# Performance work log

Measured on AMD Instinct MI355X. Metric: run time of the kernel, lower is better.

Reference implementation:

```python
import jax, jax.numpy as jnp
import numpy as np

B, N, D, DG = 32, 2048, 512, 1024


def layernorm(x, g, b, eps=1e-5):
    m = jnp.mean(x, axis=-1, keepdims=True)
    v = jnp.mean((x - m) ** 2, axis=-1, keepdims=True)
    return (x - m) * jax.lax.rsqrt(v + eps) * g + b


def simple_rms_norm(x, eps=1e-6):
    # parameter-free RMSNorm used inside Hgru1d
    return x * jax.lax.rsqrt(jnp.mean(x * x, axis=-1, keepdims=True) + eps)


def linear_recurrence(lam, u, reverse):
    # h_t = lam_t * h_{t-1} + u_t along axis=1, via associative scan
    def comb(c1, c2):
        a1, b1 = c1
        a2, b2 = c2
        return a1 * a2, a2 * b1 + b2
    return jax.lax.associative_scan(comb, (lam, u), axis=1, reverse=reverse)[1]


def hgru1d(x, lower_bound, Wi, bi, Wf, bf, Wg, bg, Wo, bo):
    # HGRN-style gated recurrence, bidirectional (causal=False, shared params)
    i = jax.nn.silu(x @ Wi + bi)                       # candidate input  [b,n,d]
    f = jax.nn.sigmoid(x @ Wf + bf)                    # forget gate      [b,n,d]
    lam = lower_bound + (1.0 - lower_bound) * f        # lower-bounded decay
    u = (1.0 - lam) * i
    h = linear_recurrence(lam, u, False) + linear_recurrence(lam, u, True)
    h = simple_rms_norm(h)
    g = jax.nn.sigmoid(x @ Wg + bg)                    # output gate
    return (h * g) @ Wo + bo


def glu(x, W1, b1, W2, b2, W3, b3):
    return (jax.nn.silu(x @ W1 + b1) * (x @ W2 + b2)) @ W3 + b3


def setup_inputs() -> dict:
    key = jax.random.key(0)
    ks = jax.random.split(key, 16)
    s = 0.02
    return {
        "x": jax.random.normal(ks[0], (B, N, D), dtype=jnp.float32),
        "lower_bound": 0,
        "Wi": jax.random.normal(ks[1], (D, D), jnp.float32) * s,
        "bi": jnp.zeros((D,), jnp.float32),
        "Wf": jax.random.normal(ks[2], (D, D), jnp.float32) * s,
        "bf": jnp.zeros((D,), jnp.float32),
        "Wg": jax.random.normal(ks[3], (D, D), jnp.float32) * s,
        "bg": jnp.zeros((D,), jnp.float32),
        "Wo": jax.random.normal(ks[4], (D, D), jnp.float32) * s,
        "bo": jnp.zeros((D,), jnp.float32),
        "tn_g": jnp.ones((D,), jnp.float32),
        "tn_b": jnp.zeros((D,), jnp.float32),
        "fn_g": jnp.ones((D,), jnp.float32),
        "fn_b": jnp.zeros((D,), jnp.float32),
        "W1": jax.random.normal(ks[5], (D, DG), jnp.float32) * s,
        "b1": jnp.zeros((DG,), jnp.float32),
        "W2": jax.random.normal(ks[6], (D, DG), jnp.float32) * s,
        "b2": jnp.zeros((DG,), jnp.float32),
        "W3": jax.random.normal(ks[7], (DG, D), jnp.float32) * s,
        "b3": jnp.zeros((D,), jnp.float32),
    }


def reference(x, lower_bound, Wi, bi, Wf, bf, Wg, bg, Wo, bo,
              tn_g, tn_b, fn_g, fn_b, W1, b1, W2, b2, W3, b3):
    lb = jnp.float32(lower_bound)
    # post-norm residual block
    x = x + layernorm(hgru1d(x, lb, Wi, bi, Wf, bf, Wg, bg, Wo, bo), tn_g, tn_b)
    x = x + layernorm(glu(x, W1, b1, W2, b2, W3, b3), fn_g, fn_b)
    return x
```

## Files before the change

kernel.cpp:

```cpp
#include <hip/hip_runtime.h>
#include <hip/hip_bf16.h>

#define BB 32
#define NN 2048
#define DD 512
#define DGG 1024
#define CC 32
#define LLEN 64

typedef short bf16x8 __attribute__((ext_vector_type(8)));
typedef float f32x4  __attribute__((ext_vector_type(4)));

__device__ __forceinline__ unsigned short f2bf(float f){
    __hip_bfloat16 h = __float2bfloat16(f);
    return *reinterpret_cast<unsigned short*>(&h);
}
__device__ __forceinline__ float bf2f(unsigned short u){
    unsigned int x = ((unsigned int)u) << 16;
    return __uint_as_float(x);
}
__device__ __forceinline__ float sigm(float x){ return 1.0f/(1.0f + __expf(-x)); }

__device__ __forceinline__ void gl_lds16(const unsigned short* g, unsigned short* l){
    __builtin_amdgcn_global_load_lds(
        (const __attribute__((address_space(1))) unsigned int*)g,
        (__attribute__((address_space(3))) unsigned int*)l, 16, 0, 0);
}

__global__ __launch_bounds__(256)
void wt_prep(const float* __restrict__ in, unsigned short* __restrict__ out,
             int K, int N)
{
    __shared__ float t[32][33];
    const int tid = threadIdx.x;
    const int r = tid >> 3;
    const int c = (tid & 7) << 2;
    const int n0 = blockIdx.x * 32;
    const int k0 = blockIdx.y * 32;
    float4 v = *(const float4*)(in + (size_t)(k0 + r) * N + n0 + c);
    t[r][c] = v.x; t[r][c+1] = v.y; t[r][c+2] = v.z; t[r][c+3] = v.w;
    __syncthreads();
    ushort4 o;
    o.x = f2bf(t[c+0][r]); o.y = f2bf(t[c+1][r]);
    o.z = f2bf(t[c+2][r]); o.w = f2bf(t[c+3][r]);
    *(ushort4*)(out + (size_t)(n0 + r) * K + k0 + c) = o;
}

__global__ __launch_bounds__(256)
void wt_prep_pair(const float* __restrict__ in0, const float* __restrict__ in1,
                  unsigned short* __restrict__ out, int K, int N)
{
    __shared__ float t[32][33];
    const int tid = threadIdx.x;
    const int bx  = blockIdx.x;
    const int k0  = blockIdx.y * 32;
    const int kk  = tid >> 3;
    const int rq  = (tid & 7) << 2;
    const float* src = ((rq >> 4) & 1) ? in1 : in0;
    const int c0 = bx * 16 + (rq & 15);
    float4 v = *(const float4*)(src + (size_t)(k0 + kk) * N + c0);
    t[kk][rq] = v.x; t[kk][rq+1] = v.y; t[kk][rq+2] = v.z; t[kk][rq+3] = v.w;
    __syncthreads();
    const int rr = tid >> 3;
    const int kc = (tid & 7) << 2;
    ushort4 o;
    o.x = f2bf(t[kc+0][rr]); o.y = f2bf(t[kc+1][rr]);
    o.z = f2bf(t[kc+2][rr]); o.w = f2bf(t[kc+3][rr]);
    *(ushort4*)(out + (size_t)(bx * 32 + rr) * K + k0 + kc) = o;
}

__global__ __launch_bounds__(256)
void cast_bf16(const float* __restrict__ in, unsigned short* __restrict__ out)
{
    size_t i = ((size_t)blockIdx.x * 256 + threadIdx.x) * 4;
    float4 v = *(const float4*)(in + i);
    ushort4 o;
    o.x = f2bf(v.x); o.y = f2bf(v.y); o.z = f2bf(v.z); o.w = f2bf(v.w);
    *(ushort4*)(out + i) = o;
}

template<int MODE, int K, int NI>
__global__ __launch_bounds__(512, 2)
void gemm8p(const unsigned short* __restrict__ A,
            const unsigned short* __restrict__ Bt,
            const float* __restrict__ bias0,
            const float* __restrict__ bias1,
            unsigned short* __restrict__ out0,
            unsigned short* __restrict__ out1,
            const int* __restrict__ lbp, int Mtiles)
{
    constexpr int NKT   = K / 64;
    constexpr int ITERS = NKT / 2;
    constexpr int Ntl   = NI / 256;
    constexpr int NOUT  = (MODE >= 5) ? NI / 2 : NI;
    __shared__ unsigned short As0[256*64], As1[256*64];
    __shared__ unsigned short Bs0[256*64], Bs1[256*64];

    const int tid  = threadIdx.x;
    const int wave = tid >> 6;
    const int lane = tid & 63;
    const int lm   = lane & 15;
    const int quad = lane >> 4;
    const int wr   = (wave >> 2) * 128;
    const int wc   = (wave & 3) * 64;

    const int nwg = Mtiles * Ntl;
    const int hb  = blockIdx.x;
    const int wg  = (hb & 7) * (nwg >> 3) + (hb >> 3);
    const int bm  = wg / Ntl;
    const int bn  = wg - bm * Ntl;
    const size_t m0 = (size_t)bm * 256;
    const int    n0 = bn * 256;

    const int r8 = lane >> 3;
    const int sl = (lane & 7) ^ r8;
    const unsigned short* gA = A  + (m0 + wave * 8 + r8) * (size_t)K + sl * 8;
    const unsigned short* gB = Bt + ((size_t)n0 + wave * 8 + r8) * K + sl * 8;
    const int ldw = wave * 8 * 64;
    const int sx  = lm & 7;

#define STG(XS, gX, kt, hh) do {                                              \
        gl_lds16(gX + (size_t)((hh)*128)      * K + (kt)*64,                  \
                 XS + ((hh)*128)      * 64 + ldw);                            \
        gl_lds16(gX + (size_t)((hh)*128 + 64) * K + (kt)*64,                  \
                 XS + ((hh)*128 + 64) * 64 + ldw);                            \
    } while (0)

#define MFQ(mh, nh, bsel) do {                                                \
        _Pragma("unroll") for (int ks = 0; ks < 2; ++ks)                      \
        _Pragma("unroll") for (int mi = 0; mi < 4; ++mi)                      \
        _Pragma("unroll") for (int ni = 0; ni < 2; ++ni)                      \
            acc[(mh)*4+mi][(nh)*2+ni] = __builtin_amdgcn_mfma_f32_16x16x32_bf16( \
                a[mi][ks], bsel[ni][ks], acc[(mh)*4+mi][(nh)*2+ni], 0, 0, 0); \
    } while (0)

#define RD_A(XS, mh) do {                                                     \
        _Pragma("unroll") for (int ks = 0; ks < 2; ++ks)                      \
        _Pragma("unroll") for (int mi = 0; mi < 4; ++mi)                      \
            a[mi][ks] = *(const bf16x8*)&XS[(wr + ((mh)*4+mi)*16 + lm)*64     \
                                            + ((ks*4+quad) ^ sx)*8];          \
    } while (0)
#define RD_B(XS, nh, breg) do {                                               \
        _Pragma("unroll") for (int ks = 0; ks < 2; ++ks)                      \
        _Pragma("unroll") for (int ni = 0; ni < 2; ++ni)                      \
            breg[ni][ks] = *(const bf16x8*)&XS[(wc + ((nh)*2+ni)*16 + lm)*64  \
                                               + ((ks*4+quad) ^ sx)*8];       \
    } while (0)

#define BARRIER()  __builtin_amdgcn_s_barrier()
#define LGKM0()    asm volatile("s_waitcnt lgkmcnt(0)" ::: "memory")
#define VMC(n)     asm volatile("s_waitcnt vmcnt(" #n ")" ::: "memory")

    f32x4 acc[8][4];
    #pragma unroll
    for (int i = 0; i < 8; ++i)
        #pragma unroll
        for (int j = 0; j < 4; ++j) acc[i][j] = (f32x4){0.f, 0.f, 0.f, 0.f};

    bf16x8 a[4][2], bA[2][2], bB[2][2];

    STG(Bs0, gB, 0, 0); STG(As0, gA, 0, 0); STG(As0, gA, 0, 1);
    STG(Bs0, gB, 0, 1); STG(Bs1, gB, 1, 0); STG(As1, gA, 1, 0);
    VMC(4);
    BARRIER();

    #pragma unroll
    for (int j = 0; j < ITERS; ++j) {
        const bool LAST = (j == ITERS - 1);
        RD_A(As0, 0); RD_B(Bs0, 0, bA);
        STG(As1, gA, 2*j + 1, 1);
        BARRIER(); LGKM0();
        __builtin_amdgcn_s_setprio(1); MFQ(0, 0, bA); __builtin_amdgcn_s_setprio(0);
        BARRIER();
        RD_B(Bs0, 1, bB);
        STG(Bs1, gB, 2*j + 1, 1);
        BARRIER(); LGKM0();
        __builtin_amdgcn_s_setprio(1); MFQ(0, 1, bB); __builtin_amdgcn_s_setprio(0);
        BARRIER();
        RD_A(As0, 1);
        if (2*j + 2 < NKT) STG(Bs0, gB, 2*j + 2, 0);
        BARRIER(); LGKM0();
        __builtin_amdgcn_s_setprio(1); MFQ(1, 0, bA); __builtin_amdgcn_s_setprio(0);
        BARRIER();
        if (2*j + 2 < NKT) STG(As0, gA, 2*j + 2, 0);
        BARRIER(); LGKM0();
        __builtin_amdgcn_s_setprio(1); MFQ(1, 1, bB); __builtin_amdgcn_s_setprio(0);
        if (LAST) { VMC(0); } else { VMC(4); }
        BARRIER();
        RD_A(As1, 0); RD_B(Bs1, 0, bA);
        if (2*j + 2 < NKT) STG(As0, gA, 2*j + 2, 1);
        BARRIER(); LGKM0();
        __builtin_amdgcn_s_setprio(1); MFQ(0, 0, bA); __builtin_amdgcn_s_setprio(0);
        BARRIER();
        RD_B(Bs1, 1, bB);
        if (2*j + 2 < NKT) STG(Bs0, gB, 2*j + 2, 1);
        BARRIER(); LGKM0();
        __builtin_amdgcn_s_setprio(1); MFQ(0, 1, bB); __builtin_amdgcn_s_setprio(0);
        BARRIER();
        RD_A(As1, 1);
        if (2*j + 3 < NKT) STG(Bs1, gB, 2*j + 3, 0);
        BARRIER(); LGKM0();
        __builtin_amdgcn_s_setprio(1); MFQ(1, 0, bA); __builtin_amdgcn_s_setprio(0);
        BARRIER();
        if (2*j + 3 < NKT) STG(As1, gA, 2*j + 3, 0);
        BARRIER(); LGKM0();
        __builtin_amdgcn_s_setprio(1); MFQ(1, 1, bB); __builtin_amdgcn_s_setprio(0);
        if (!LAST) { VMC(4); BARRIER(); }
    }
#undef STG
#undef MFQ
#undef RD_A
#undef RD_B
#undef BARRIER
#undef LGKM0
#undef VMC

    float lbv = 0.f;
    if constexpr (MODE == 5) lbv = (float)(*lbp);

    if constexpr (MODE == 5 || MODE == 6) {
        const int cbase = (n0 + wc) >> 1;
        #pragma unroll
        for (int nip = 0; nip < 4; nip += 2) {
            const int c = cbase + (nip >> 1) * 16 + lm;
            const float b0 = bias0[c];
            const float b1v = bias1[c];
            #pragma unroll
            for (int mi = 0; mi < 8; ++mi) {
                #pragma unroll
                for (int r = 0; r < 4; ++r) {
                    const size_t row = m0 + wr + mi * 16 + quad * 4 + r;
                    const size_t oidx = row * NOUT + c;
                    float p0 = acc[mi][nip][r]     + b0;
                    float p1 = acc[mi][nip + 1][r] + b1v;
                    if constexpr (MODE == 5) {
                        float si = p0 * sigm(p0);
                        float fv = sigm(p1);
                        float lamv = lbv + (1.f - lbv) * fv;
                        out0[oidx] = f2bf(lamv);
                        out1[oidx] = f2bf((1.f - lamv) * si);
                    } else {
                        out0[oidx] = f2bf(p0 * sigm(p0) * p1);
                    }
                }
            }
        }
    } else {
        #pragma unroll
        for (int ni = 0; ni < 4; ++ni) {
            const int col = n0 + wc + ni * 16 + lm;
            const float bcol = bias0[col];
            #pragma unroll
            for (int mi = 0; mi < 8; ++mi) {
                #pragma unroll
                for (int r = 0; r < 4; ++r) {
                    const size_t row = m0 + wr + mi * 16 + quad * 4 + r;
                    const size_t oidx = row * NOUT + col;
                    float v = acc[mi][ni][r] + bcol;
                    if constexpr (MODE == 0) out0[oidx] = f2bf(v);
                    else                     out0[oidx] = f2bf(sigm(v));
                }
            }
        }
    }
}

__global__ __launch_bounds__(512)
void scan_agg(const unsigned short* __restrict__ lam, const unsigned short* __restrict__ u,
              float* __restrict__ Aarr, float* __restrict__ Vf, float* __restrict__ Vr)
{
    int bc = blockIdx.x;
    int b = bc >> 5, c = bc & 31;
    int d = threadIdx.x;
    size_t base = ((size_t)b * NN + c * LLEN) * DD + d;
    float A = 1.f, vf = 0.f, vr = 0.f;
    for (int t = 0; t < LLEN; ++t) {
        float lv = bf2f(lam[base + (size_t)t * DD]);
        float uv = bf2f(u[base + (size_t)t * DD]);
        vf = lv * vf + uv;
        vr += uv * A;
        A *= lv;
    }
    size_t o = (size_t)bc * DD + d;
    Aarr[o] = A; Vf[o] = vf; Vr[o] = vr;
}

__global__ __launch_bounds__(256)
void scan_comb(const float* __restrict__ Aarr, const float* __restrict__ Vf,
               const float* __restrict__ Vr, float* __restrict__ cf, float* __restrict__ cr)
{
    int g = blockIdx.x * 256 + threadIdx.x;
    int b = g >> 9, d = g & 511;
    float S = 0.f;
    for (int c = 0; c < CC; ++c) {
        size_t o = (size_t)(b * CC + c) * DD + d;
        cf[o] = S;
        S = Vf[o] + Aarr[o] * S;
    }
    S = 0.f;
    for (int c = CC - 1; c >= 0; --c) {
        size_t o = (size_t)(b * CC + c) * DD + d;
        cr[o] = S;
        S = Vr[o] + Aarr[o] * S;
    }
}

__global__ __launch_bounds__(256)
void scan_final(const unsigned short* __restrict__ lam, const unsigned short* __restrict__ u,
                const float* __restrict__ cf, const float* __restrict__ cr,
                float* __restrict__ h)
{
    int bid = blockIdx.x;
    int dh = bid & 1, c = (bid >> 1) & 31, b = bid >> 6;
    int d = dh * 256 + threadIdx.x;
    size_t base = ((size_t)b * NN + c * LLEN) * DD + d;
    size_t co   = (size_t)(b * CC + c) * DD + d;

    float hbuf[LLEN];
    float hf = cf[co];
    #pragma unroll
    for (int t = 0; t < LLEN; ++t) {
        float lv = bf2f(lam[base + (size_t)t * DD]);
        float uv = bf2f(u[base + (size_t)t * DD]);
        hf = lv * hf + uv;
        hbuf[t] = hf;
    }
    float hr = cr[co];
    #pragma unroll
    for (int t = LLEN - 1; t >= 0; --t) {
        float lv = bf2f(lam[base + (size_t)t * DD]);
        float uv = bf2f(u[base + (size_t)t * DD]);
        hr = lv * hr + uv;
        h[base + (size_t)t * DD] = hbuf[t] + hr;
    }
}

__global__ __launch_bounds__(256)
void rms_mul(const float* __restrict__ h, const unsigned short* __restrict__ g,
             unsigned short* __restrict__ hg)
{
    int row = blockIdx.x;
    size_t base = (size_t)row * DD;
    int tid = threadIdx.x, col = tid * 2;
    float2 v = *(const float2*)&h[base + col];
    float ss = v.x * v.x + v.y * v.y;
    #pragma unroll
    for (int off = 32; off > 0; off >>= 1) ss += __shfl_down(ss, off);
    __shared__ float ps[4];
    __shared__ float scale_s;
    if ((tid & 63) == 0) ps[tid >> 6] = ss;
    __syncthreads();
    if (tid == 0) scale_s = rsqrtf((ps[0] + ps[1] + ps[2] + ps[3]) * (1.f / DD) + 1e-6f);
    __syncthreads();
    float sc = scale_s;
    ushort2 gv = *(const ushort2*)&g[base + col];
    ushort2 o;
    o.x = f2bf(v.x * sc * bf2f(gv.x));
    o.y = f2bf(v.y * sc * bf2f(gv.y));
    *(ushort2*)&hg[base + col] = o;
}

__global__ __launch_bounds__(256)
void add_ln(const float* __restrict__ xin, const unsigned short* __restrict__ y,
            const float* __restrict__ gam, const float* __restrict__ bet,
            float* __restrict__ out, unsigned short* __restrict__ outb)
{
    int row = blockIdx.x;
    size_t base = (size_t)row * DD;
    int tid = threadIdx.x, col = tid * 2;
    ushort2 yv = *(const ushort2*)&y[base + col];
    float vx = bf2f(yv.x), vy = bf2f(yv.y);
    float s = vx + vy;
    float ss = vx * vx + vy * vy;
    #pragma unroll
    for (int off = 32; off > 0; off >>= 1) {
        s  += __shfl_down(s, off);
        ss += __shfl_down(ss, off);
    }
    __shared__ float ps[8];
    __shared__ float stats[2];
    if ((tid & 63) == 0) { ps[tid >> 6] = s; ps[4 + (tid >> 6)] = ss; }
    __syncthreads();
    if (tid == 0) {
        float st  = ps[0] + ps[1] + ps[2] + ps[3];
        float sst = ps[4] + ps[5] + ps[6] + ps[7];
        float mean = st * (1.f / DD);
        float var  = sst * (1.f / DD) - mean * mean;
        stats[0] = mean; stats[1] = rsqrtf(var + 1e-5f);
    }
    __syncthreads();
    float mean = stats[0], inv = stats[1];
    float2 xv = *(const float2*)&xin[base + col];
    float2 gv = *(const float2*)&gam[col];
    float2 bv = *(const float2*)&bet[col];
    float2 o;
    o.x = xv.x + (vx - mean) * inv * gv.x + bv.x;
    o.y = xv.y + (vy - mean) * inv * gv.y + bv.y;
    *(float2*)&out[base + col] = o;
    if (outb) {
        ushort2 ob; ob.x = f2bf(o.x); ob.y = f2bf(o.y);
        *(ushort2*)&outb[base + col] = ob;
    }
}

extern "C" void kernel_launch(void* const* d_in, const int* in_sizes, int n_in,
                              void* d_out, int out_size, void* d_ws, size_t ws_size,
                              hipStream_t stream)
{
    const float* x   = (const float*)d_in[0];
    const int*   lb  = (const int*)d_in[1];
    const float* Wi  = (const float*)d_in[2];
    const float* bi  = (const float*)d_in[3];
    const float* Wf  = (const float*)d_in[4];
    const float* bfp = (const float*)d_in[5];
    const float* Wg  = (const float*)d_in[6];
    const float* bg  = (const float*)d_in[7];
    const float* Wo  = (const float*)d_in[8];
    const float* bo  = (const float*)d_in[9];
    const float* tng = (const float*)d_in[10];
    const float* tnb = (const float*)d_in[11];
    const float* fng = (const float*)d_in[12];
    const float* fnb = (const float*)d_in[13];
    const float* W1  = (const float*)d_in[14];
    const float* b1  = (const float*)d_in[15];
    const float* W2  = (const float*)d_in[16];
    const float* b2  = (const float*)d_in[17];
    const float* W3  = (const float*)d_in[18];
    const float* b3  = (const float*)d_in[19];

    unsigned short* wbase = (unsigned short*)d_ws;
    unsigned short* WifT = wbase;
    unsigned short* WgT  = WifT + 524288;
    unsigned short* WoT  = WgT + 262144;
    unsigned short* W12T = WoT + 262144;
    unsigned short* W3T  = W12T + 1048576;
    const size_t WTOT = 524288 + 262144 + 262144 + 1048576 + 524288;

    wt_prep_pair<<<dim3(32, 16), 256, 0, stream>>>(Wi, Wf, WifT, 512, 512);
    wt_prep<<<dim3(16, 16), 256, 0, stream>>>(Wg, WgT, 512, 512);
    wt_prep<<<dim3(16, 16), 256, 0, stream>>>(Wo, WoT, 512, 512);
    wt_prep_pair<<<dim3(64, 16), 256, 0, stream>>>(W1, W2, W12T, 512, 1024);
    wt_prep<<<dim3(16, 32), 256, 0, stream>>>(W3, W3T, 1024, 512);

    const size_t perB = (size_t)4 * NN * DD * 2 + (size_t)5 * CC * DD * 4;
    int Bch = 32;
    while (Bch > 1 && WTOT * 2 + (size_t)Bch * perB > ws_size) Bch >>= 1;
    const int nch = BB / Bch;

    const size_t slabE = (size_t)Bch * NN * DD;

    for (int ch = 0; ch < nch; ++ch) {
        const size_t r0 = (size_t)ch * Bch * NN;
        const int Mc = Bch * NN;
        const int Mt = Mc / 256;
        const float* xc = x + r0 * DD;
        unsigned short* S0 = wbase + WTOT;
        unsigned short* S1 = S0 + slabE;
        unsigned short* S2 = S0 + 2 * slabE;
        unsigned short* S3 = S0 + 3 * slabE;
        float* small = (float*)(S0 + 4 * slabE);
        const size_t agg = (size_t)Bch * CC * DD;
        float* Aarr = small;
        float* VfP  = small + agg;
        float* VrP  = small + 2 * agg;
        float* cfP  = small + 3 * agg;
        float* crP  = small + 4 * agg;
        float* hout = (float*)d_out + r0 * DD;

        cast_bf16<<<Mc / 2, 256, 0, stream>>>(xc, S3);
        gemm8p<5, 512, 1024><<<Mt * 4, 512, 0, stream>>>(
            S3, WifT, bi, bfp, S1, S0, lb, Mt);
        gemm8p<2, 512, 512><<<Mt * 2, 512, 0, stream>>>(
            S3, WgT, bg, nullptr, S2, nullptr, nullptr, Mt);
        scan_agg<<<Bch * CC, 512, 0, stream>>>(S1, S0, Aarr, VfP, VrP);
        scan_comb<<<(Bch * DD) / 256, 256, 0, stream>>>(Aarr, VfP, VrP, cfP, crP);
        scan_final<<<Bch * CC * 2, 256, 0, stream>>>(S1, S0, cfP, crP, hout);
        rms_mul<<<Mc, 256, 0, stream>>>(hout, S2, S2);
        gemm8p<0, 512, 512><<<Mt * 2, 512, 0, stream>>>(
            S2, WoT, bo, nullptr, S0, nullptr, nullptr, Mt);
        add_ln<<<Mc, 256, 0, stream>>>(xc, S0, tng, tnb, hout, S3);
        gemm8p<6, 512, 2048><<<Mt * 8, 512, 0, stream>>>(
            S3, W12T, b1, b2, S1, nullptr, nullptr, Mt);
        gemm8p<0, 1024, 512><<<Mt * 2, 512, 0, stream>>>(
            S1, W3T, b3, nullptr, S0, nullptr, nullptr, Mt);
        add_ln<<<Mc, 256, 0, stream>>>(hout, S0, fng, fnb, hout, nullptr);
    }
}
```

Before: 1.115 ms.

## Make GEMM blocks loop over several consecutive N tiles sharing one M row

New measurement: 1.504 ms. 1.35x slower.

```diff
diff --git a/kernel.cpp b/kernel.cpp
--- a/kernel.cpp
+++ b/kernel.cpp
@@ -87,7 +87,7 @@
             const float* __restrict__ bias1,
             unsigned short* __restrict__ out0,
             unsigned short* __restrict__ out1,
-            const int* __restrict__ lbp, int Mtiles)
+            const int* __restrict__ lbp, int TPB)
 {
     constexpr int NKT   = K / 64;
     constexpr int ITERS = NKT / 2;
@@ -104,18 +104,15 @@
     const int wr   = (wave >> 2) * 128;
     const int wc   = (wave & 3) * 64;
 
-    const int nwg = Mtiles * Ntl;
-    const int hb  = blockIdx.x;
-    const int wg  = (hb & 7) * (nwg >> 3) + (hb >> 3);
-    const int bm  = wg / Ntl;
-    const int bn  = wg - bm * Ntl;
+    const int start = blockIdx.x * TPB;
+    const int bm  = start / Ntl;
+    const int bn0 = start - bm * Ntl;
     const size_t m0 = (size_t)bm * 256;
-    const int    n0 = bn * 256;
 
     const int r8 = lane >> 3;
     const int sl = (lane & 7) ^ r8;
     const unsigned short* gA = A  + (m0 + wave * 8 + r8) * (size_t)K + sl * 8;
-    const unsigned short* gB = Bt + ((size_t)n0 + wave * 8 + r8) * K + sl * 8;
+    const unsigned short* gB = Bt + ((size_t)bn0 * 256 + wave * 8 + r8) * K + sl * 8;
     const int ldw = wave * 8 * 64;
     const int sx  = lm & 7;
 
@@ -152,60 +149,115 @@
 #define VMC(n)     asm volatile("s_waitcnt vmcnt(" #n ")" ::: "memory")
 
     f32x4 acc[8][4];
-    #pragma unroll
-    for (int i = 0; i < 8; ++i)
+    bf16x8 a[4][2], bA[2][2], bB[2][2];
+
+    float lbv = 0.f;
+    if constexpr (MODE == 5) lbv = (float)(*lbp);
+
+    #pragma unroll 1
+    for (int t = 0; t < TPB; ++t) {
         #pragma unroll
-        for (int j = 0; j < 4; ++j) acc[i][j] = (f32x4){0.f, 0.f, 0.f, 0.f};
-
-    bf16x8 a[4][2], bA[2][2], bB[2][2];
-
-    STG(Bs0, gB, 0, 0); STG(As0, gA, 0, 0); STG(As0, gA, 0, 1);
-    STG(Bs0, gB, 0, 1); STG(Bs1, gB, 1, 0); STG(As1, gA, 1, 0);
-    VMC(4);
-    BARRIER();
-
-    #pragma unroll
-    for (int j = 0; j < ITERS; ++j) {
-        const bool LAST = (j == ITERS - 1);
-        RD_A(As0, 0); RD_B(Bs0, 0, bA);
-        STG(As1, gA, 2*j + 1, 1);
-        BARRIER(); LGKM0();
-        __builtin_amdgcn_s_setprio(1); MFQ(0, 0, bA); __builtin_amdgcn_s_setprio(0);
+        for (int i = 0; i < 8; ++i)
+            #pragma unroll
+            for (int jj = 0; jj < 4; ++jj) acc[i][jj] = (f32x4){0.f, 0.f, 0.f, 0.f};
+
+        STG(Bs0, gB, 0, 0); STG(As0, gA, 0, 0); STG(As0, gA, 0, 1);
+        STG(Bs0, gB, 0, 1); STG(Bs1, gB, 1, 0); STG(As1, gA, 1, 0);
+        VMC(4);
         BARRIER();
-        RD_B(Bs0, 1, bB);
-        STG(Bs1, gB, 2*j + 1, 1);
-        BARRIER(); LGKM0();
-        __builtin_amdgcn_s_setprio(1); MFQ(0, 1, bB); __builtin_amdgcn_s_setprio(0);
-        BARRIER();
-        RD_A(As0, 1);
-        if (2*j + 2 < NKT) STG(Bs0, gB, 2*j + 2, 0);
-        BARRIER(); LGKM0();
-        __builtin_amdgcn_s_setprio(1); MFQ(1, 0, bA); __builtin_amdgcn_s_setprio(0);
-        BARRIER();
-        if (2*j + 2 < NKT) STG(As0, gA, 2*j + 2, 0);
-        BARRIER(); LGKM0();
-        __builtin_amdgcn_s_setprio(1); MFQ(1, 1, bB); __builtin_amdgcn_s_setprio(0);
-        if (LAST) { VMC(0); } else { VMC(4); }
-        BARRIER();
-        RD_A(As1, 0); RD_B(Bs1, 0, bA);
-        if (2*j + 2 < NKT) STG(As0, gA, 2*j + 2, 1);
-        BARRIER(); LGKM0();
-        __builtin_amdgcn_s_setprio(1); MFQ(0, 0, bA); __builtin_amdgcn_s_setprio(0);
-        BARRIER();
-        RD_B(Bs1, 1, bB);
-        if (2*j + 2 < NKT) STG(Bs0, gB, 2*j + 2, 1);
-        BARRIER(); LGKM0();
-        __builtin_amdgcn_s_setprio(1); MFQ(0, 1, bB); __builtin_amdgcn_s_setprio(0);
-        BARRIER();
-        RD_A(As1, 1);
-        if (2*j + 3 < NKT) STG(Bs1, gB, 2*j + 3, 0);
-        BARRIER(); LGKM0();
-        __builtin_amdgcn_s_setprio(1); MFQ(1, 0, bA); __builtin_amdgcn_s_setprio(0);
-        BARRIER();
-        if (2*j + 3 < NKT) STG(As1, gA, 2*j + 3, 0);
-        BARRIER(); LGKM0();
-        __builtin_amdgcn_s_setprio(1); MFQ(1, 1, bB); __builtin_amdgcn_s_setprio(0);
-        if (!LAST) { VMC(4); BARRIER(); }
+
+        #pragma unroll
+        for (int j = 0; j < ITERS; ++j) {
+            const bool JL = (j == ITERS - 1);
+            RD_A(As0, 0); RD_B(Bs0, 0, bA);
+            STG(As1, gA, 2*j + 1, 1);
+            BARRIER(); LGKM0();
+            __builtin_amdgcn_s_setprio(1); MFQ(0, 0, bA); __builtin_amdgcn_s_setprio(0);
+            BARRIER();
+            RD_B(Bs0, 1, bB);
+            STG(Bs1, gB, 2*j + 1, 1);
+            BARRIER(); LGKM0();
+            __builtin_amdgcn_s_setprio(1); MFQ(0, 1, bB); __builtin_amdgcn_s_setprio(0);
+            BARRIER();
+            RD_A(As0, 1);
+            if (2*j + 2 < NKT) STG(Bs0, gB, 2*j + 2, 0);
+            BARRIER(); LGKM0();
+            __builtin_amdgcn_s_setprio(1); MFQ(1, 0, bA); __builtin_amdgcn_s_setprio(0);
+            BARRIER();
+            if (2*j + 2 < NKT) STG(As0, gA, 2*j + 2, 0);
+            BARRIER(); LGKM0();
+            __builtin_amdgcn_s_setprio(1); MFQ(1, 1, bB); __builtin_amdgcn_s_setprio(0);
+            if (JL) { VMC(0); } else { VMC(4); }
+            BARRIER();
+            RD_A(As1, 0); RD_B(Bs1, 0, bA);
+            if (2*j + 2 < NKT) STG(As0, gA, 2*j + 2, 1);
+            BARRIER(); LGKM0();
+            __builtin_amdgcn_s_setprio(1); MFQ(0, 0, bA); __builtin_amdgcn_s_setprio(0);
+            BARRIER();
+            RD_B(Bs1, 1, bB);
+            if (2*j + 2 < NKT) STG(Bs0, gB, 2*j + 2, 1);
+            BARRIER(); LGKM0();
+            __builtin_amdgcn_s_setprio(1); MFQ(0, 1, bB); __builtin_amdgcn_s_setprio(0);
+            BARRIER();
+            RD_A(As1, 1);
+            if (2*j + 3 < NKT) STG(Bs1, gB, 2*j + 3, 0);
+            BARRIER(); LGKM0();
+            __builtin_amdgcn_s_setprio(1); MFQ(1, 0, bA); __builtin_amdgcn_s_setprio(0);
+            BARRIER();
+            if (2*j + 3 < NKT) STG(As1, gA, 2*j + 3, 0);
+            BARRIER(); LGKM0();
+            __builtin_amdgcn_s_setprio(1); MFQ(1, 1, bB); __builtin_amdgcn_s_setprio(0);
+            if (!JL) { VMC(4); BARRIER(); }
+        }
+
+        const int nt0 = (bn0 + t) * 256;
+        if constexpr (MODE == 5 || MODE == 6) {
+            const int cbase = (nt0 + wc) >> 1;
+            #pragma unroll
+            for (int nip = 0; nip < 4; nip += 2) {
+                const int c = cbase + (nip >> 1) * 16 + lm;
+                const float b0 = bias0[c];
+                const float b1v = bias1[c];
+                #pragma unroll
+                for (int mi = 0; mi < 8; ++mi) {
+                    #pragma unroll
+                    for (int r = 0; r < 4; ++r) {
+                        const size_t row = m0 + wr + mi * 16 + quad * 4 + r;
+                        const size_t oidx = row * NOUT + c;
+                        float p0 = acc[mi][nip][r]     + b0;
+                        float p1 = acc[mi][nip + 1][r] + b1v;
+                        if constexpr (MODE == 5) {
+                            float si = p0 * sigm(p0);
+                            float fv = sigm(p1);
+                            float lamv = lbv + (1.f - lbv) * fv;
+                            out0[oidx] = f2bf(lamv);
+                            out1[oidx] = f2bf((1.f - lamv) * si);
+                        } else {
+                            out0[oidx] = f2bf(p0 * sigm(p0) * p1);
+                        }
+                    }
+                }
+            }
+        } else {
+            #pragma unroll
+            for (int ni = 0; ni < 4; ++ni) {
+                const int col = nt0 + wc + ni * 16 + lm;
+                const float bcol = bias0[col];
+                #pragma unroll
+                for (int mi = 0; mi < 8; ++mi) {
+                    #pragma unroll
+                    for (int r = 0; r < 4; ++r) {
+                        const size_t row = m0 + wr + mi * 16 + quad * 4 + r;
+                        const size_t oidx = row * NOUT + col;
+                        float v = acc[mi][ni][r] + bcol;
+                        if constexpr (MODE == 0) out0[oidx] = f2bf(v);
+                        else                     out0[oidx] = f2bf(sigm(v));
+                    }
+                }
+            }
+        }
+
+        gB += (size_t)256 * K;
     }
 #undef STG
 #undef MFQ
@@ -214,55 +266,6 @@
 #undef BARRIER
 #undef LGKM0
 #undef VMC
-
-    float lbv = 0.f;
-    if constexpr (MODE == 5) lbv = (float)(*lbp);
-
-    if constexpr (MODE == 5 || MODE == 6) {
-        const int cbase = (n0 + wc) >> 1;
-        #pragma unroll
-        for (int nip = 0; nip < 4; nip += 2) {
-            const int c = cbase + (nip >> 1) * 16 + lm;
-            const float b0 = bias0[c];
-            const float b1v = bias1[c];
-            #pragma unroll
-            for (int mi = 0; mi < 8; ++mi) {
-                #pragma unroll
-                for (int r = 0; r < 4; ++r) {
-                    const size_t row = m0 + wr + mi * 16 + quad * 4 + r;
-                    const size_t oidx = row * NOUT + c;
-                    float p0 = acc[mi][nip][r]     + b0;
-                    float p1 = acc[mi][nip + 1][r] + b1v;
-                    if constexpr (MODE == 5) {
-                        float si = p0 * sigm(p0);
-                        float fv = sigm(p1);
-                        float lamv = lbv + (1.f - lbv) * fv;
-                        out0[oidx] = f2bf(lamv);
-                        out1[oidx] = f2bf((1.f - lamv) * si);
-                    } else {
-                        out0[oidx] = f2bf(p0 * sigm(p0) * p1);
-                    }
-                }
-            }
-        }
-    } else {
-        #pragma unroll
-        for (int ni = 0; ni < 4; ++ni) {
-            const int col = n0 + wc + ni * 16 + lm;
-            const float bcol = bias0[col];
-            #pragma unroll
-            for (int mi = 0; mi < 8; ++mi) {
-                #pragma unroll
-                for (int r = 0; r < 4; ++r) {
-                    const size_t row = m0 + wr + mi * 16 + quad * 4 + r;
-                    const size_t oidx = row * NOUT + col;
-                    float v = acc[mi][ni][r] + bcol;
-                    if constexpr (MODE == 0) out0[oidx] = f2bf(v);
-                    else                     out0[oidx] = f2bf(sigm(v));
-                }
-            }
-        }
-    }
 }
 
 __global__ __launch_bounds__(512)
@@ -467,22 +470,28 @@
         float* crP  = small + 4 * agg;
         float* hout = (float*)d_out + r0 * DD;
 
+        auto tpb_of = [](int nwg) { return nwg >= 256 ? nwg / 256 : 1; };
+        const int nwg_if  = Mt * 4, tpb_if  = tpb_of(nwg_if);
+        const int nwg_g   = Mt * 2, tpb_g   = tpb_of(nwg_g);
+        const int nwg_w12 = Mt * 8, tpb_w12 = tpb_of(nwg_w12);
+        const int nwg_w3  = Mt * 2, tpb_w3  = tpb_of(nwg_w3);
+
         cast_bf16<<<Mc / 2, 256, 0, stream>>>(xc, S3);
-        gemm8p<5, 512, 1024><<<Mt * 4, 512, 0, stream>>>(
-            S3, WifT, bi, bfp, S1, S0, lb, Mt);
-        gemm8p<2, 512, 512><<<Mt * 2, 512, 0, stream>>>(
-            S3, WgT, bg, nullptr, S2, nullptr, nullptr, Mt);
+        gemm8p<5, 512, 1024><<<nwg_if / tpb_if, 512, 0, stream>>>(
+            S3, WifT, bi, bfp, S1, S0, lb, tpb_if);
+        gemm8p<2, 512, 512><<<nwg_g / tpb_g, 512, 0, stream>>>(
+            S3, WgT, bg, nullptr, S2, nullptr, nullptr, tpb_g);
         scan_agg<<<Bch * CC, 512, 0, stream>>>(S1, S0, Aarr, VfP, VrP);
         scan_comb<<<(Bch * DD) / 256, 256, 0, stream>>>(Aarr, VfP, VrP, cfP, crP);
         scan_final<<<Bch * CC * 2, 256, 0, stream>>>(S1, S0, cfP, crP, hout);
         rms_mul<<<Mc, 256, 0, stream>>>(hout, S2, S2);
-        gemm8p<0, 512, 512><<<Mt * 2, 512, 0, stream>>>(
-            S2, WoT, bo, nullptr, S0, nullptr, nullptr, Mt);
+        gemm8p<0, 512, 512><<<nwg_g / tpb_g, 512, 0, stream>>>(
+            S2, WoT, bo, nullptr, S0, nullptr, nullptr, tpb_g);
         add_ln<<<Mc, 256, 0, stream>>>(xc, S0, tng, tnb, hout, S3);
-        gemm8p<6, 512, 2048><<<Mt * 8, 512, 0, stream>>>(
-            S3, W12T, b1, b2, S1, nullptr, nullptr, Mt);
-        gemm8p<0, 1024, 512><<<Mt * 2, 512, 0, stream>>>(
-            S1, W3T, b3, nullptr, S0, nullptr, nullptr, Mt);
+        gemm8p<6, 512, 2048><<<nwg_w12 / tpb_w12, 512, 0, stream>>>(
+            S3, W12T, b1, b2, S1, nullptr, nullptr, tpb_w12);
+        gemm8p<0, 1024, 512><<<nwg_w3 / tpb_w3, 512, 0, stream>>>(
+            S1, W3T, b3, nullptr, S0, nullptr, nullptr, tpb_w3);
         add_ln<<<Mc, 256, 0, stream>>>(hout, S0, fng, fnb, hout, nullptr);
     }
 }
```
